# Kernel tuning notes

Measured on AMD Instinct MI355X. Metric: run time of the kernel, lower is better.

## Reference

```python
import jax, jax.numpy as jnp
import numpy as np

HIDDEN = 1024
ORDER = 3
OS_FACTOR = 1.5
INPUT = 512
B = 64
T = 512


def lagrange_kernel(delta: float, order: int) -> jnp.ndarray:
    kern = np.ones(order + 1, dtype=np.float64)
    for n in range(order + 1):
        for k in range(order + 1):
            if k != n:
                kern[n] *= (delta - k) / (n - k)
    return jnp.asarray(kern, dtype=jnp.float32)


def setup_inputs() -> dict:
    key = jax.random.key(0)
    ks = jax.random.split(key, 5)
    s_ih = 1.0 / np.sqrt(HIDDEN)
    return {
        "x": jax.random.normal(ks[0], (B, T, INPUT), dtype=jnp.float32),
        "W_ih": jax.random.normal(ks[1], (4 * HIDDEN, INPUT), dtype=jnp.float32) * s_ih,
        "W_hh": jax.random.normal(ks[2], (4 * HIDDEN, HIDDEN), dtype=jnp.float32) * s_ih,
        "b_ih": jax.random.normal(ks[3], (4 * HIDDEN,), dtype=jnp.float32) * s_ih,
        "b_hh": jax.random.normal(ks[4], (4 * HIDDEN,), dtype=jnp.float32) * s_ih,
    }


def reference(x, W_ih, W_hh, b_ih, b_hh):
    # os_factor=1.5 < 2  ->  delta = 0.5, epsilon = 1  (write index i-eps+1 == i)
    delta = OS_FACTOR - 1.0
    kernel = lagrange_kernel(delta, ORDER)            # [order+1]
    state_size = 2 * HIDDEN
    prev0 = jnp.zeros((B, ORDER + 1, state_size), dtype=x.dtype)

    def step(prev_states, xi):
        # Lagrange-interpolated state read: [B, 2H]
        h_read = jnp.einsum('k,bks->bs', kernel, prev_states)
        h_prev, c_prev = h_read[:, :HIDDEN], h_read[:, HIDDEN:]
        gates = xi @ W_ih.T + b_ih + h_prev @ W_hh.T + b_hh  # [B, 4H]
        i_g, f_g, g_g, o_g = jnp.split(gates, 4, axis=-1)    # torch gate order i,f,g,o
        c = jax.nn.sigmoid(f_g) * c_prev + jax.nn.sigmoid(i_g) * jnp.tanh(g_g)
        h = jax.nn.sigmoid(o_g) * jnp.tanh(c)
        hc = jnp.concatenate([h, c], axis=-1)                 # [B, 2H]
        # prev_states[-1] = detached new state, then roll(shifts=1) -> new state at front
        new_prev = jnp.concatenate(
            [jax.lax.stop_gradient(hc)[:, None, :], prev_states[:, :-1]], axis=1)
        return new_prev, hc

    _, states = jax.lax.scan(step, prev0, jnp.swapaxes(x, 0, 1))  # states: [T, B, 2H]
    states = jnp.swapaxes(states, 0, 1)                           # [B, T, 2H]
    return states[..., :HIDDEN], states[:, -1, :]
```

## Files before the change

### kernel.cpp

```cpp
#include <hip/hip_runtime.h>

#define BATCH   64
#define SEQT    512
#define NIN     512
#define NH      1024
#define NG      4096

typedef __attribute__((ext_vector_type(8))) short short8;
typedef __attribute__((ext_vector_type(4))) float floatx4;

__device__ __forceinline__ float bf2f(unsigned short u) {
    union { float f; unsigned i; } v; v.i = ((unsigned)u) << 16; return v.f;
}
__device__ __forceinline__ unsigned short f2bf(float f) {
    union { float f; unsigned i; } v; v.f = f;
    unsigned x = v.i;
    unsigned r = (x + 0x7fffu + ((x >> 16) & 1u)) >> 16;
    return (unsigned short)r;
}
__device__ __forceinline__ float fsigm(float x) {
    return __builtin_amdgcn_rcpf(1.0f + __expf(-x));
}
__device__ __forceinline__ float ftanh(float x) {
    return 1.0f - 2.0f * __builtin_amdgcn_rcpf(1.0f + __expf(2.0f * x));
}

__global__ void cvt_bf16(const float* __restrict__ src, unsigned short* __restrict__ dst, long n) {
    long i = (long)blockIdx.x * blockDim.x + threadIdx.x;
    long stride = (long)gridDim.x * blockDim.x;
    for (; i < n; i += stride) dst[i] = f2bf(src[i]);
}

__global__ void prep_whh(const float* __restrict__ W, unsigned short* __restrict__ dst) {
    long i = (long)blockIdx.x * blockDim.x + threadIdx.x;
    if (i >= (long)NG * NH) return;
    int cs  = (int)(i & (NH - 1));
    int row = (int)(i >> 10) & 63;
    int rg  = (int)(i >> 16);
    int c   = cs ^ ((row & 7) << 3);
    int g = row >> 4, nl = row & 15;
    long src = ((long)(g * NH + rg * 16 + nl) << 10) + c;
    dst[i] = f2bf(W[src]);
}

__global__ __launch_bounds__(256) void gemm_ih(const unsigned short* __restrict__ A,
                                               const unsigned short* __restrict__ Wb,
                                               const float* __restrict__ b_ih,
                                               const float* __restrict__ b_hh,
                                               unsigned short* __restrict__ G) {
    __shared__ __align__(16) unsigned short a_lds[128][56];
    __shared__ __align__(16) unsigned short b_lds[128][56];
    const int tid  = threadIdx.x;
    const int lane = tid & 63;
    const int w    = tid >> 6;
    const int wm   = w >> 1, wn = w & 1;
    const int bm   = blockIdx.x, bn = blockIdx.y;

    floatx4 acc[4][4] = {};

    const int row = tid >> 1, seg = tid & 1;
    const unsigned short* gA = A  + ((size_t)(bm * 128 + row)) * NIN + seg * 16;
    const unsigned short* gB = Wb + ((size_t)(bn * 128 + row)) * NIN + seg * 16;

    for (int kt = 0; kt < 16; ++kt) {
        __syncthreads();
        *(uint4*)&a_lds[row][seg * 16]     = *(const uint4*)(gA + kt * 32);
        *(uint4*)&a_lds[row][seg * 16 + 8] = *(const uint4*)(gA + kt * 32 + 8);
        *(uint4*)&b_lds[row][seg * 16]     = *(const uint4*)(gB + kt * 32);
        *(uint4*)&b_lds[row][seg * 16 + 8] = *(const uint4*)(gB + kt * 32 + 8);
        __syncthreads();
        short8 af[4], bf[4];
#pragma unroll
        for (int mt = 0; mt < 4; ++mt)
            af[mt] = *(const short8*)&a_lds[wm * 64 + mt * 16 + (lane & 15)][(lane >> 4) * 8];
#pragma unroll
        for (int nt = 0; nt < 4; ++nt)
            bf[nt] = *(const short8*)&b_lds[wn * 64 + nt * 16 + (lane & 15)][(lane >> 4) * 8];
#pragma unroll
        for (int mt = 0; mt < 4; ++mt)
#pragma unroll
            for (int nt = 0; nt < 4; ++nt)
                acc[mt][nt] = __builtin_amdgcn_mfma_f32_16x16x32_bf16(af[mt], bf[nt], acc[mt][nt], 0, 0, 0);
    }
#pragma unroll
    for (int nt = 0; nt < 4; ++nt) {
        int n = bn * 128 + wn * 64 + nt * 16 + (lane & 15);
        float bias = b_ih[n] + b_hh[n];
#pragma unroll
        for (int mt = 0; mt < 4; ++mt) {
#pragma unroll
            for (int r = 0; r < 4; ++r) {
                int m = bm * 128 + wm * 64 + mt * 16 + (lane >> 4) * 4 + r;
                int b = m >> 9, t = m & 511;
                size_t gi = ((size_t)(t * 64 + b)) * NG + n;
                G[gi] = f2bf(acc[mt][nt][r] + bias);
            }
        }
    }
}

__global__ __launch_bounds__(256, 1) void seq_kernel(const unsigned short* __restrict__ Wp,
                                                     const unsigned short* __restrict__ G,
                                                     unsigned short* __restrict__ hread,
                                                     unsigned* __restrict__ flags,
                                                     float* __restrict__ out) {
    const int tid  = threadIdx.x;
    const int lane = tid & 63;
    const int w    = tid >> 6;
    const int bid  = blockIdx.x;
    const int bg   = bid & 3;
    const int rg   = bid >> 2;

    __shared__ __align__(16) unsigned short w_lds[64 * 1024];
    __shared__ float part[4][16][68];

    {
        const unsigned short* src = Wp + (size_t)rg * 65536;
#pragma unroll 4
        for (int u = 0; u < 32; ++u)
            *(uint4*)&w_lds[u * 2048 + tid * 8] = *(const uint4*)(src + u * 2048 + tid * 8);
    }
    __syncthreads();

    const int cb = tid >> 4;
    const int nl = tid & 15;
    const int b  = bg * 16 + cb;
    const int u  = rg * 16 + nl;

    float h0 = 0.f, h1 = 0.f, h2 = 0.f, h3 = 0.f;
    float c0 = 0.f, c1 = 0.f, c2 = 0.f, c3 = 0.f;
    float c_read = 0.f;

    const unsigned short* Gp = G + (size_t)b * NG + u;
    float* out_h = out + (size_t)b * SEQT * NH + u;

    const size_t pub_idx = ((size_t)((rg >> 1) * 64 + ((rg & 1) * 2 + (nl >> 3)) * 16 + cb)) * 8 + (nl & 7);
    const int swz   = (lane & 7) << 3;
    const int brow0 = lane & 15;
    const int kofs  = (lane >> 4) * 8;
    const unsigned* fwave = flags + bg * 64 + w * 16 + (lane & 15);

    for (int t = 0; t < SEQT; ++t) {
        const unsigned short* Gt = Gp + (size_t)t * 64 * NG;
        unsigned short gi_u = Gt[0], gf_u = Gt[1024], gg_u = Gt[2048], go_u = Gt[3072];

        if (t > 0) {
            while (!__all((int)(__hip_atomic_load(fwave, __ATOMIC_RELAXED, __HIP_MEMORY_SCOPE_AGENT) >= (unsigned)t)))
                __builtin_amdgcn_s_sleep(1);
            asm volatile("" ::: "memory");
        }

        const size_t abase = (size_t)(t & 1) * 65536 + (size_t)bg * 16384;
        const unsigned long long* hp = (const unsigned long long*)(hread + abase)
                                       + ((size_t)w * 512 + lane) * 2;
        unsigned long long aq[16];
#pragma unroll
        for (int kk = 0; kk < 8; ++kk) {
            aq[kk * 2]     = __hip_atomic_load(hp + kk * 128,     __ATOMIC_RELAXED, __HIP_MEMORY_SCOPE_AGENT);
            aq[kk * 2 + 1] = __hip_atomic_load(hp + kk * 128 + 1, __ATOMIC_RELAXED, __HIP_MEMORY_SCOPE_AGENT);
        }
        floatx4 acc[4] = {};
#pragma unroll
        for (int kk = 0; kk < 8; ++kk) {
            union { unsigned long long q[2]; short8 v; } au;
            au.q[0] = aq[kk * 2]; au.q[1] = aq[kk * 2 + 1];
            const int cbase = ((w * 8 + kk) * 32 + kofs) ^ swz;
#pragma unroll
            for (int nt = 0; nt < 4; ++nt) {
                short8 bfr = *(const short8*)&w_lds[(nt * 16 + brow0) * 1024 + cbase];
                acc[nt] = __builtin_amdgcn_mfma_f32_16x16x32_bf16(au.v, bfr, acc[nt], 0, 0, 0);
            }
        }
#pragma unroll
        for (int nt = 0; nt < 4; ++nt)
#pragma unroll
            for (int r = 0; r < 4; ++r)
                part[w][(lane >> 4) * 4 + r][nt * 16 + (lane & 15)] = acc[nt][r];
        __syncthreads();

        float gi = (part[0][cb][nl]      + part[1][cb][nl])      + (part[2][cb][nl]      + part[3][cb][nl]);
        float gf = (part[0][cb][16 + nl] + part[1][cb][16 + nl]) + (part[2][cb][16 + nl] + part[3][cb][16 + nl]);
        float gg = (part[0][cb][32 + nl] + part[1][cb][32 + nl]) + (part[2][cb][32 + nl] + part[3][cb][32 + nl]);
        float go = (part[0][cb][48 + nl] + part[1][cb][48 + nl]) + (part[2][cb][48 + nl] + part[3][cb][48 + nl]);
        gi += bf2f(gi_u); gf += bf2f(gf_u); gg += bf2f(gg_u); go += bf2f(go_u);

        float c = fsigm(gf) * c_read + fsigm(gi) * ftanh(gg);
        float h = fsigm(go) * ftanh(c);

        h3 = h2; h2 = h1; h1 = h0; h0 = h;
        c3 = c2; c2 = c1; c1 = c0; c0 = c;
        float hr = 0.3125f * h0 + 0.9375f * h1 - 0.3125f * h2 + 0.0625f * h3;
        c_read   = 0.3125f * c0 + 0.9375f * c1 - 0.3125f * c2 + 0.0625f * c3;

        {
            unsigned v  = (unsigned)f2bf(hr);
            unsigned p0 = v | (__shfl_xor(v, 1) << 16);
            unsigned p2 = __shfl_xor(p0, 2);
            if ((nl & 3) == 0) {
                unsigned long long q = (unsigned long long)p0 | ((unsigned long long)p2 << 32);
                unsigned long long* dst = (unsigned long long*)(hread
                    + (size_t)((t + 1) & 1) * 65536 + (size_t)bg * 16384 + pub_idx);
                __hip_atomic_store(dst, q, __ATOMIC_RELAXED, __HIP_MEMORY_SCOPE_AGENT);
            }
        }

        __syncthreads();
        if (tid == 0)
            __hip_atomic_store(&flags[bg * 64 + rg], (unsigned)(t + 1), __ATOMIC_RELAXED, __HIP_MEMORY_SCOPE_AGENT);

        out_h[(size_t)t * NH] = h;
        if (t == SEQT - 1) {
            float* o2 = out + (size_t)BATCH * SEQT * NH + (size_t)b * 2 * NH;
            o2[u] = h;
            o2[NH + u] = c;
        }
    }
}

extern "C" void kernel_launch(void* const* d_in, const int* in_sizes, int n_in,
                              void* d_out, int out_size, void* d_ws, size_t ws_size,
                              hipStream_t stream) {
    const float* x    = (const float*)d_in[0];
    const float* Wih  = (const float*)d_in[1];
    const float* Whh  = (const float*)d_in[2];
    const float* bih  = (const float*)d_in[3];
    const float* bhh  = (const float*)d_in[4];
    float* outp = (float*)d_out;

    char* ws = (char*)d_ws;
    unsigned short* xb    = (unsigned short*)(ws);
    unsigned short* wihb  = (unsigned short*)(ws + 33554432);
    unsigned short* whhb  = (unsigned short*)(ws + 37748736);
    unsigned short* G     = (unsigned short*)(ws + 46137344);
    unsigned short* hread = (unsigned short*)(ws + 314572800);
    unsigned*       flags = (unsigned*)(ws + 314834944);

    hipMemsetAsync(hread, 0, 262144 + 1024, stream);

    cvt_bf16<<<4096, 256, 0, stream>>>(x, xb, (long)BATCH * SEQT * NIN);
    cvt_bf16<<<2048, 256, 0, stream>>>(Wih, wihb, (long)NG * NIN);
    prep_whh<<<16384, 256, 0, stream>>>(Whh, whhb);
    gemm_ih<<<dim3(256, 32), 256, 0, stream>>>(xb, wihb, bih, bhh, G);

    void* args[] = { (void*)&whhb, (void*)&G, (void*)&hread, (void*)&flags, (void*)&outp };
    hipLaunchCooperativeKernel((void*)seq_kernel, dim3(256), dim3(256), args, 0, stream);
}
```

Baseline: 2.332 ms.

## Replace per-step flag barrier with tagged h-state words carrying step numbers

The separate per-block flag array and its spin-wait are removed. Each published 64-bit word now packs two bf16 hidden values with the step index in the high half, so consumers poll the data words directly and retry until every tag matches. This drops one global round-trip (flag store, flag poll, then data load) and the block barrier before the flag store on the recurrent critical path. The cost is twice the bytes loaded and stored per step. The hq buffer reuses the workspace region of wihb after gemm_ih has finished, and is zeroed just before the sequential kernel.

Result: slower. 2.793 ms (+19.8%).

```diff
diff --git a/kernel.cpp b/kernel.cpp
--- a/kernel.cpp
+++ b/kernel.cpp
@@ -101,8 +101,7 @@
 
 __global__ __launch_bounds__(256, 1) void seq_kernel(const unsigned short* __restrict__ Wp,
                                                      const unsigned short* __restrict__ G,
-                                                     unsigned short* __restrict__ hread,
-                                                     unsigned* __restrict__ flags,
+                                                     unsigned long long* __restrict__ hq,
                                                      float* __restrict__ out) {
     const int tid  = threadIdx.x;
     const int lane = tid & 63;
@@ -134,36 +133,45 @@
     const unsigned short* Gp = G + (size_t)b * NG + u;
     float* out_h = out + (size_t)b * SEQT * NH + u;
 
-    const size_t pub_idx = ((size_t)((rg >> 1) * 64 + ((rg & 1) * 2 + (nl >> 3)) * 16 + cb)) * 8 + (nl & 7);
+    unsigned long long* hq0 = hq + (size_t)bg * 8192;
+    unsigned long long* hq1 = hq + 32768 + (size_t)bg * 8192;
+
+    const int qidx = ((rg >> 1) * 64 + ((rg & 1) * 2 + (nl >> 3)) * 16 + cb) * 4 + ((nl & 7) >> 1);
+
     const int swz   = (lane & 7) << 3;
     const int brow0 = lane & 15;
     const int kofs  = (lane >> 4) * 8;
-    const unsigned* fwave = flags + bg * 64 + w * 16 + (lane & 15);
 
     for (int t = 0; t < SEQT; ++t) {
         const unsigned short* Gt = Gp + (size_t)t * 64 * NG;
         unsigned short gi_u = Gt[0], gf_u = Gt[1024], gg_u = Gt[2048], go_u = Gt[3072];
 
-        if (t > 0) {
-            while (!__all((int)(__hip_atomic_load(fwave, __ATOMIC_RELAXED, __HIP_MEMORY_SCOPE_AGENT) >= (unsigned)t)))
-                __builtin_amdgcn_s_sleep(1);
-            asm volatile("" ::: "memory");
-        }
-
-        const size_t abase = (size_t)(t & 1) * 65536 + (size_t)bg * 16384;
-        const unsigned long long* hp = (const unsigned long long*)(hread + abase)
-                                       + ((size_t)w * 512 + lane) * 2;
-        unsigned long long aq[16];
+        const unsigned long long* hp = ((t & 1) ? hq1 : hq0)
+                                       + (size_t)w * 2048 + (size_t)lane * 4;
+        unsigned long long q[32];
+        for (int retry = 0; retry < 16384; ++retry) {
+#pragma unroll
+            for (int kk = 0; kk < 8; ++kk)
+#pragma unroll
+                for (int s = 0; s < 4; ++s)
+                    q[kk * 4 + s] = __hip_atomic_load(hp + kk * 256 + s,
+                                                      __ATOMIC_RELAXED, __HIP_MEMORY_SCOPE_AGENT);
+            if (t == 0) break;
+            unsigned acc_t = 0;
+#pragma unroll
+            for (int i = 0; i < 32; ++i)
+                acc_t |= (unsigned)(q[i] >> 32) ^ (unsigned)t;
+            if (acc_t == 0) break;
+            __builtin_amdgcn_s_sleep(2);
+        }
+
+        floatx4 acc[4] = {};
 #pragma unroll
         for (int kk = 0; kk < 8; ++kk) {
-            aq[kk * 2]     = __hip_atomic_load(hp + kk * 128,     __ATOMIC_RELAXED, __HIP_MEMORY_SCOPE_AGENT);
-            aq[kk * 2 + 1] = __hip_atomic_load(hp + kk * 128 + 1, __ATOMIC_RELAXED, __HIP_MEMORY_SCOPE_AGENT);
-        }
-        floatx4 acc[4] = {};
-#pragma unroll
-        for (int kk = 0; kk < 8; ++kk) {
-            union { unsigned long long q[2]; short8 v; } au;
-            au.q[0] = aq[kk * 2]; au.q[1] = aq[kk * 2 + 1];
+            union { unsigned uw[4]; short8 v; } au;
+#pragma unroll
+            for (int s = 0; s < 4; ++s)
+                au.uw[s] = (unsigned)q[kk * 4 + s];
             const int cbase = ((w * 8 + kk) * 32 + kofs) ^ swz;
 #pragma unroll
             for (int nt = 0; nt < 4; ++nt) {
@@ -193,20 +201,15 @@
         c_read   = 0.3125f * c0 + 0.9375f * c1 - 0.3125f * c2 + 0.0625f * c3;
 
         {
-            unsigned v  = (unsigned)f2bf(hr);
-            unsigned p0 = v | (__shfl_xor(v, 1) << 16);
-            unsigned p2 = __shfl_xor(p0, 2);
-            if ((nl & 3) == 0) {
-                unsigned long long q = (unsigned long long)p0 | ((unsigned long long)p2 << 32);
-                unsigned long long* dst = (unsigned long long*)(hread
-                    + (size_t)((t + 1) & 1) * 65536 + (size_t)bg * 16384 + pub_idx);
-                __hip_atomic_store(dst, q, __ATOMIC_RELAXED, __HIP_MEMORY_SCOPE_AGENT);
+            unsigned hv = (unsigned)f2bf(hr);
+            unsigned p0 = hv | (__shfl_xor(hv, 1) << 16);
+            if ((nl & 1) == 0) {
+                unsigned long long qv = ((unsigned long long)(unsigned)(t + 1) << 32)
+                                        | (unsigned long long)p0;
+                __hip_atomic_store(((t & 1) ? hq0 : hq1) + qidx, qv,
+                                   __ATOMIC_RELAXED, __HIP_MEMORY_SCOPE_AGENT);
             }
         }
-
-        __syncthreads();
-        if (tid == 0)
-            __hip_atomic_store(&flags[bg * 64 + rg], (unsigned)(t + 1), __ATOMIC_RELAXED, __HIP_MEMORY_SCOPE_AGENT);
 
         out_h[(size_t)t * NH] = h;
         if (t == SEQT - 1) {
@@ -214,6 +217,10 @@
             o2[u] = h;
             o2[NH + u] = c;
         }
+
+        __builtin_amdgcn_sched_barrier(0);
+        __builtin_amdgcn_s_barrier();
+        __builtin_amdgcn_sched_barrier(0);
     }
 }
 
@@ -232,16 +239,15 @@
     unsigned short* wihb  = (unsigned short*)(ws + 33554432);
     unsigned short* whhb  = (unsigned short*)(ws + 37748736);
     unsigned short* G     = (unsigned short*)(ws + 46137344);
-    unsigned short* hread = (unsigned short*)(ws + 314572800);
-    unsigned*       flags = (unsigned*)(ws + 314834944);
-
-    hipMemsetAsync(hread, 0, 262144 + 1024, stream);
+    unsigned long long* hq = (unsigned long long*)(ws + 33554432);
 
     cvt_bf16<<<4096, 256, 0, stream>>>(x, xb, (long)BATCH * SEQT * NIN);
     cvt_bf16<<<2048, 256, 0, stream>>>(Wih, wihb, (long)NG * NIN);
     prep_whh<<<16384, 256, 0, stream>>>(Whh, whhb);
     gemm_ih<<<dim3(256, 32), 256, 0, stream>>>(xb, wihb, bih, bhh, G);
 
-    void* args[] = { (void*)&whhb, (void*)&G, (void*)&hread, (void*)&flags, (void*)&outp };
+    hipMemsetAsync(hq, 0, 524288, stream);
+
+    void* args[] = { (void*)&whhb, (void*)&G, (void*)&hq, (void*)&outp };
     hipLaunchCooperativeKernel((void*)seq_kernel, dim3(256), dim3(256), args, 0, stream);
 }
```
